# Kernel tuning notes

Hardware: AMD Instinct MI355X
Metric: run time of the kernel (lower is better)

## Reference

```python
import jax, jax.numpy as jnp
import numpy as np

B, N_P, N_S, D, H = 8, 512, 512, 512, 8
HD = D // H
SCALE = HD ** -0.5


def setup_inputs() -> dict:
    key = jax.random.key(0)
    ks = jax.random.split(key, 16)
    init = lambda k, shape, fan_in: jax.random.normal(k, shape, jnp.float32) * (1.0 / np.sqrt(fan_in))
    return {
        "piece_embeds": jax.random.normal(ks[0], (B, N_P, D), jnp.float32),
        "slot_embeds": jax.random.normal(ks[1], (B, N_S, D), jnp.float32),
        "mask": jax.random.randint(ks[2], (B, N_P, N_S), 0, 2, jnp.int32),
        "spatial_bias": jax.random.normal(ks[3], (B, N_P, N_S), jnp.float32),
        "Wq": init(ks[4], (D, D), D), "bq": jnp.zeros((D,), jnp.float32),
        "Wk": init(ks[5], (D, D), D), "bk": jnp.zeros((D,), jnp.float32),
        "Wv": init(ks[6], (D, D), D), "bv": jnp.zeros((D,), jnp.float32),
        "Wo": init(ks[7], (D, D), D), "bo": jnp.zeros((D,), jnp.float32),
        "Wc": init(ks[8], (2 * D,), 2 * D), "bc": jnp.zeros((), jnp.float32),
        "Wval": init(ks[9], (D,), D), "bval": jnp.zeros((), jnp.float32),
    }


def reference(piece_embeds, slot_embeds, mask, spatial_bias,
              Wq, bq, Wk, bk, Wv, bv, Wo, bo, Wc, bc, Wval, bval):
    Bv, Np, Dv = piece_embeds.shape
    Ns = slot_embeds.shape[1]
    Q = (piece_embeds @ Wq + bq).reshape(Bv, Np, H, HD)
    K = (slot_embeds @ Wk + bk).reshape(Bv, Ns, H, HD)
    V = (slot_embeds @ Wv + bv).reshape(Bv, Ns, H, HD)
    # per-head scores, scaled, then averaged over heads (non-standard)
    scores = jnp.einsum('bphd,bshd->bps', Q, K) * (SCALE / H)
    scores = scores + spatial_bias
    scores = jnp.where(mask == 0, jnp.float32(-1e9), scores)
    attn_probs = jax.nn.softmax(scores, axis=-1)  # dropout is identity at eval
    # the original expand*mul*sum over [B,Np,Ns,H,HD] == this contraction
    attn_output = jnp.einsum('bps,bshd->bphd', attn_probs, V).reshape(Bv, Np, Dv)
    output = attn_output @ Wo + bo
    value = (output.mean(axis=1) @ Wval + bval)[:, None]  # [B,1]
    # concat-linear over pairs == split-weight GEMMs with broadcast add
    Wc_p, Wc_s = Wc[:Dv], Wc[Dv:]
    compatibility = (piece_embeds @ Wc_p)[:, :, None] + (slot_embeds @ Wc_s)[:, None, :] + bc
    return scores, value, compatibility
```

## Files before the change

### kernel.cpp

```cpp
#include <hip/hip_runtime.h>
#include <math.h>

#define NP 512
#define NS 512
#define DD 512
#define INV64 0.015625f
#define NEGBIG -1000000000.0f
#define LOG2E 1.4426950408889634f

#define WS_MTBF   0
#define WS_TBF    131072
#define WS_PBF    1179648
#define WS_SBF    2228224
#define WS_WQBF   3276800
#define WS_WKBF   3407872
#define WS_WV     3538944
#define WS_U      3539456
#define WS_WQBK   3539968
#define WS_WKBQ   3540480
#define WS_VV     3540992
#define WS_A      3545088
#define WS_E      3549184
#define WS_CP     3553280
#define WS_CS     3557376
#define WS_Z      3561472
#define WS_W      3565568
#define WS_SC     3569664
#define WS_CNT    3569680

#define OUT_SCORES 0
#define OUT_VALUE  2097152
#define OUT_COMP   2097160

typedef short bf16x8 __attribute__((ext_vector_type(8)));
typedef float f32x4 __attribute__((ext_vector_type(4)));

__device__ __forceinline__ short f2bf(float f) {
  unsigned u = __builtin_bit_cast(unsigned, f);
  u += 0x7fffu + ((u >> 16) & 1u);
  return (short)(u >> 16);
}

__device__ __forceinline__ void async_copy16(const void* g, void* l) {
  __builtin_amdgcn_global_load_lds(
      (const __attribute__((address_space(1))) unsigned int*)g,
      (__attribute__((address_space(3))) unsigned int*)l, 16, 0, 0);
}

__device__ __forceinline__ float dot8(float4 a0, float4 a1, float4 b0, float4 b1) {
  return a0.x * b0.x + a0.y * b0.y + a0.z * b0.z + a0.w * b0.w +
         a1.x * b1.x + a1.y * b1.y + a1.z * b1.z + a1.w * b1.w;
}

__device__ __forceinline__ float wave_red(float s) {
#pragma unroll
  for (int o = 32; o; o >>= 1) s += __shfl_xor(s, o);
  return s;
}

__device__ inline float wave_dot512(const float* __restrict__ x,
                                    const float* __restrict__ y, int lane) {
  float4 x0 = *(const float4*)&x[lane * 8];
  float4 x1 = *(const float4*)&x[lane * 8 + 4];
  float4 y0 = *(const float4*)&y[lane * 8];
  float4 y1 = *(const float4*)&y[lane * 8 + 4];
  return wave_red(dot8(x0, x1, y0, y1));
}

__global__ __launch_bounds__(256) void kA(
    const float* __restrict__ Wo, const float* __restrict__ Wval,
    const float* __restrict__ Wq, const float* __restrict__ bk,
    const float* __restrict__ Wk, const float* __restrict__ bq,
    const float* __restrict__ bo, const float* __restrict__ bval,
    float* __restrict__ ws, short* __restrict__ wqb, short* __restrict__ wkb) {
  int blk = blockIdx.x;
  if (blk < 385) {
    int wid = blk * 4 + (threadIdx.x >> 6);
    int lane = threadIdx.x & 63;
    if (wid >= 1538) return;
    const float *x, *y;
    float* dst;
    float extra = 0.f;
    int r = wid & 511;
    if (wid < 512)        { x = Wo + (size_t)r * DD; y = Wval; dst = ws + WS_WV + r; }
    else if (wid < 1024)  { x = Wq + (size_t)r * DD; y = bk;   dst = ws + WS_WQBK + r; }
    else if (wid < 1536)  { x = Wk + (size_t)r * DD; y = bq;   dst = ws + WS_WKBQ + r; }
    else if (wid == 1536) { x = bo; y = Wval; dst = ws + WS_SC + 1; extra = *bval; }
    else                  { x = bq; y = bk;   dst = ws + WS_SC + 2; }
    float s = wave_dot512(x, y, lane);
    if (lane == 0) *dst = s + extra;
  } else {
    int t = (blk - 385) * 256 + threadIdx.x;
    const float* src;
    short* dst;
    int off;
    if (t < 32768) { src = Wq; dst = wqb; off = t * 8; }
    else           { src = Wk; dst = wkb; off = (t - 32768) * 8; }
    float4 v0 = *(const float4*)&src[off];
    float4 v1 = *(const float4*)&src[off + 4];
    bf16x8 o;
    o[0] = f2bf(v0.x); o[1] = f2bf(v0.y); o[2] = f2bf(v0.z); o[3] = f2bf(v0.w);
    o[4] = f2bf(v1.x); o[5] = f2bf(v1.y); o[6] = f2bf(v1.z); o[7] = f2bf(v1.w);
    *(bf16x8*)&dst[off] = o;
  }
}

template <int MODE>
__global__ __launch_bounds__(256) void k64(
    const short* __restrict__ A, const short* __restrict__ B,
    short* __restrict__ Cb, const float* __restrict__ Wv,
    const float* __restrict__ bv, float* __restrict__ ws,
    const float* __restrict__ sbias, const int* __restrict__ maskp,
    const float* __restrict__ bc, float* __restrict__ out) {
  __shared__ alignas(16) short SH[4][4096];
  __shared__ unsigned tick;
  const int wave = threadIdx.x >> 6, lane = threadIdx.x & 63;
  const int id = blockIdx.x;

  if (MODE == 0 && id >= 64) {
    int wid = (id - 64) * 4 + wave;
    if (wid > 512) return;
    if (wid < 512) {
      float s = wave_dot512(Wv + (size_t)wid * DD, ws + WS_WV, lane);
      if (lane == 0) ws[WS_U + wid] = s;
    } else {
      float s = wave_dot512(bv, ws + WS_WV, lane);
      if (lane == 0) ws[WS_SC + 0] = s;
    }
    return;
  }

  const int wr = wave >> 1, wc = wave & 1;
  const int li = lane & 15, g = lane >> 4;
  int b = 0, m0, n0;
  if (MODE == 0)      { m0 = (id & 7) * 64; n0 = (id >> 3) * 64; }
  else if (MODE == 1) { m0 = (id & 63) * 64; n0 = (id >> 6) * 64; }
  else                { b = id & 7; m0 = ((id >> 6) & 7) * 64; n0 = ((id >> 3) & 7) * 64; }
  const short* Ab = A + (size_t)b * NP * DD;
  const short* Bb = B + (size_t)b * NS * DD;
  f32x4 acc[2][2] = {};
  float4 sb4r[4];
  int4 mk4r[4];
  const int er = threadIdx.x >> 2, eq = threadIdx.x & 3;
  const size_t ebase = ((size_t)b * NP + m0 + er) * NS + n0 + eq * 16;

  auto stage = [&](int bufi, int k0) {
#pragma unroll
    for (int h = 0; h < 2; ++h) {
      int s = h * 256 + threadIdx.x;
      int row = s >> 3;
      int gsrc = (s & 7) ^ (row & 7);
      async_copy16(Ab + (size_t)(m0 + row) * DD + k0 + gsrc * 8, &SH[bufi][s * 8]);
      async_copy16(Bb + (size_t)(n0 + row) * DD + k0 + gsrc * 8, &SH[2 + bufi][s * 8]);
    }
  };

  stage(0, 0);
  __syncthreads();
  int buf = 0;
  for (int k0 = 0; k0 < DD; k0 += 64) {
    if (k0 + 64 < DD) stage(buf ^ 1, k0 + 64);
    if (MODE == 2) {
      if (k0 == 256) {
#pragma unroll
        for (int h = 0; h < 4; ++h)
          sb4r[h] = *(const float4*)&sbias[ebase + h * 4];
      } else if (k0 == 384) {
#pragma unroll
        for (int h = 0; h < 4; ++h)
          mk4r[h] = *(const int4*)&maskp[ebase + h * 4];
      }
    }
    bf16x8 af[2][2], bfv[2][2];
#pragma unroll
    for (int kk = 0; kk < 2; ++kk) {
#pragma unroll
      for (int am = 0; am < 2; ++am) {
        int row = wr * 32 + am * 16 + li;
        af[am][kk] = *(const bf16x8*)&SH[buf][(row * 8 + ((kk * 4 + g) ^ (row & 7))) * 8];
      }
#pragma unroll
      for (int bn = 0; bn < 2; ++bn) {
        int row = wc * 32 + bn * 16 + li;
        bfv[bn][kk] = *(const bf16x8*)&SH[2 + buf][(row * 8 + ((kk * 4 + g) ^ (row & 7))) * 8];
      }
    }
#pragma unroll
    for (int kk = 0; kk < 2; ++kk)
#pragma unroll
      for (int am = 0; am < 2; ++am)
#pragma unroll
        for (int bn = 0; bn < 2; ++bn)
          acc[am][bn] = __builtin_amdgcn_mfma_f32_16x16x32_bf16(
              af[am][kk], bfv[bn][kk], acc[am][bn], 0, 0, 0);
    if (k0 + 64 < DD) {
      __syncthreads();
      buf ^= 1;
    }
  }
  __syncthreads();

  if (MODE != 2) {
    short* cs = &SH[0][0];
#pragma unroll
    for (int am = 0; am < 2; ++am)
#pragma unroll
      for (int i = 0; i < 4; ++i) {
        int row = wr * 32 + am * 16 + g * 4 + i;
#pragma unroll
        for (int bn = 0; bn < 2; ++bn)
          cs[row * 68 + wc * 32 + bn * 16 + li] = f2bf(acc[am][bn][i]);
      }
    __syncthreads();
    int r = threadIdx.x >> 2, q = threadIdx.x & 3;
#pragma unroll
    for (int h = 0; h < 2; ++h) {
      bf16x8 v = *(const bf16x8*)&cs[r * 68 + q * 16 + h * 8];
      *(bf16x8*)&Cb[(size_t)(m0 + r) * DD + n0 + q * 16 + h * 8] = v;
    }
  } else {
    float* cf = (float*)&SH[0][0];
#pragma unroll
    for (int am = 0; am < 2; ++am)
#pragma unroll
      for (int i = 0; i < 4; ++i) {
        int row = wr * 32 + am * 16 + g * 4 + i;
#pragma unroll
        for (int bn = 0; bn < 2; ++bn)
          cf[row * 68 + wc * 32 + bn * 16 + li] = acc[am][bn][i];
      }
    __syncthreads();
    const float sbb = ws[WS_SC + 2];
    const float bcv = *bc;
    int p = m0 + er;
    float av = ws[WS_A + b * NP + p] + sbb;
    float cpv = ws[WS_CP + b * NP + p] + bcv;
    float zp = 0.f, wp = 0.f;
#pragma unroll
    for (int h = 0; h < 4; ++h) {
      int c = eq * 16 + h * 4;
      int scol = n0 + c;
      size_t idx = ebase + h * 4;
      float4 a4 = *(const float4*)&cf[er * 68 + c];
      float4 sb4 = sb4r[h];
      int4 mk4 = mk4r[h];
      float4 e4 = *(const float4*)&ws[WS_E + b * NS + scol];
      float4 vv4 = *(const float4*)&ws[WS_VV + b * NS + scol];
      float4 cs4 = *(const float4*)&ws[WS_CS + b * NS + scol];
      float4 v;
      v.x = (mk4.x == 0) ? NEGBIG : fmaf(a4.x + av + e4.x, INV64, sb4.x);
      v.y = (mk4.y == 0) ? NEGBIG : fmaf(a4.y + av + e4.y, INV64, sb4.y);
      v.z = (mk4.z == 0) ? NEGBIG : fmaf(a4.z + av + e4.z, INV64, sb4.z);
      v.w = (mk4.w == 0) ? NEGBIG : fmaf(a4.w + av + e4.w, INV64, sb4.w);
      *(float4*)&out[OUT_SCORES + idx] = v;
      float e;
      e = exp2f(v.x * LOG2E); zp += e; wp += e * vv4.x;
      e = exp2f(v.y * LOG2E); zp += e; wp += e * vv4.y;
      e = exp2f(v.z * LOG2E); zp += e; wp += e * vv4.z;
      e = exp2f(v.w * LOG2E); zp += e; wp += e * vv4.w;
      float4 cm = make_float4(cpv + cs4.x, cpv + cs4.y, cpv + cs4.z, cpv + cs4.w);
      *(float4*)&out[OUT_COMP + idx] = cm;
    }
    zp += __shfl_xor(zp, 1); zp += __shfl_xor(zp, 2);
    wp += __shfl_xor(wp, 1); wp += __shfl_xor(wp, 2);
    if (eq == 0) {
      atomicAdd(&ws[WS_Z + b * NP + p], zp);
      atomicAdd(&ws[WS_W + b * NP + p], wp);
    }
    __syncthreads();
    if (threadIdx.x == 0)
      tick = atomicAdd((unsigned*)(ws + WS_CNT) + (b * 8 + ((id >> 6) & 7)), 1u);
    __syncthreads();
    if (tick == 7 && threadIdx.x < 64) {
      int pr = m0 + threadIdx.x;
      float zz = atomicAdd(&ws[WS_Z + b * NP + pr], 0.0f);
      float ww = atomicAdd(&ws[WS_W + b * NP + pr], 0.0f);
      float v = wave_red(ww / zz);
      if (threadIdx.x == 0) atomicAdd(&out[OUT_VALUE + b], v * (1.0f / NP));
    }
  }
}

__global__ __launch_bounds__(256) void kC(
    const float* __restrict__ piece, const float* __restrict__ slot,
    const float* __restrict__ Wc, float* __restrict__ ws,
    short* __restrict__ pbf, short* __restrict__ sbf, float* __restrict__ out) {
  int lane = threadIdx.x & 63;
  if (blockIdx.x < 1024) {
    int wid = blockIdx.x * 4 + (threadIdx.x >> 6);
    const float* row = piece + (size_t)wid * DD;
    float4 x0 = *(const float4*)&row[lane * 8];
    float4 x1 = *(const float4*)&row[lane * 8 + 4];
    bf16x8 o;
    o[0] = f2bf(x0.x); o[1] = f2bf(x0.y); o[2] = f2bf(x0.z); o[3] = f2bf(x0.w);
    o[4] = f2bf(x1.x); o[5] = f2bf(x1.y); o[6] = f2bf(x1.z); o[7] = f2bf(x1.w);
    *(bf16x8*)&pbf[(size_t)wid * DD + lane * 8] = o;
    const float* y = ws + WS_WQBK;
    float4 y0 = *(const float4*)&y[lane * 8];
    float4 y1 = *(const float4*)&y[lane * 8 + 4];
    float4 c0 = *(const float4*)&Wc[lane * 8];
    float4 c1 = *(const float4*)&Wc[lane * 8 + 4];
    float da = wave_red(dot8(x0, x1, y0, y1));
    float dc = wave_red(dot8(x0, x1, c0, c1));
    if (lane == 0) { ws[WS_A + wid] = da; ws[WS_CP + wid] = dc; }
  } else if (blockIdx.x < 2048) {
    int wid = (blockIdx.x - 1024) * 4 + (threadIdx.x >> 6);
    const float* row = slot + (size_t)wid * DD;
    float4 x0 = *(const float4*)&row[lane * 8];
    float4 x1 = *(const float4*)&row[lane * 8 + 4];
    bf16x8 o;
    o[0] = f2bf(x0.x); o[1] = f2bf(x0.y); o[2] = f2bf(x0.z); o[3] = f2bf(x0.w);
    o[4] = f2bf(x1.x); o[5] = f2bf(x1.y); o[6] = f2bf(x1.z); o[7] = f2bf(x1.w);
    *(bf16x8*)&sbf[(size_t)wid * DD + lane * 8] = o;
    const float* y = ws + WS_WKBQ;
    float4 y0 = *(const float4*)&y[lane * 8];
    float4 y1 = *(const float4*)&y[lane * 8 + 4];
    const float* u = ws + WS_U;
    float4 u0 = *(const float4*)&u[lane * 8];
    float4 u1 = *(const float4*)&u[lane * 8 + 4];
    const float* c = Wc + DD;
    float4 c0 = *(const float4*)&c[lane * 8];
    float4 c1 = *(const float4*)&c[lane * 8 + 4];
    float de = wave_red(dot8(x0, x1, y0, y1));
    float dv = wave_red(dot8(x0, x1, u0, u1));
    float dc = wave_red(dot8(x0, x1, c0, c1));
    if (lane == 0) {
      ws[WS_E + wid] = de;
      ws[WS_VV + wid] = dv + ws[WS_SC + 0];
      ws[WS_CS + wid] = dc;
    }
  } else {
    float4 zz = make_float4(0.f, 0.f, 0.f, 0.f);
#pragma unroll
    for (int k = 0; k < 8; ++k)
      *(float4*)&ws[WS_Z + (threadIdx.x * 8 + k) * 4] = zz;
    if (threadIdx.x < 64) ((unsigned*)(ws + WS_CNT))[threadIdx.x] = 0u;
    if (threadIdx.x < 8) out[OUT_VALUE + threadIdx.x] = ws[WS_SC + 1];
  }
}

extern "C" void kernel_launch(void* const* d_in, const int* in_sizes, int n_in,
                              void* d_out, int out_size, void* d_ws,
                              size_t ws_size, hipStream_t stream) {
  const float* piece = (const float*)d_in[0];
  const float* slot = (const float*)d_in[1];
  const int* mask = (const int*)d_in[2];
  const float* sbias = (const float*)d_in[3];
  const float* Wq = (const float*)d_in[4];
  const float* bq = (const float*)d_in[5];
  const float* Wk = (const float*)d_in[6];
  const float* bk = (const float*)d_in[7];
  const float* Wv = (const float*)d_in[8];
  const float* bv = (const float*)d_in[9];
  const float* Wo = (const float*)d_in[10];
  const float* bo = (const float*)d_in[11];
  const float* Wc = (const float*)d_in[12];
  const float* bc = (const float*)d_in[13];
  const float* Wval = (const float*)d_in[14];
  const float* bval = (const float*)d_in[15];
  float* out = (float*)d_out;
  float* ws = (float*)d_ws;

  short* mtb = (short*)(ws + WS_MTBF);
  short* tbf = (short*)(ws + WS_TBF);
  short* pbf = (short*)(ws + WS_PBF);
  short* sbf = (short*)(ws + WS_SBF);
  short* wqb = (short*)(ws + WS_WQBF);
  short* wkb = (short*)(ws + WS_WKBF);

  hipLaunchKernelGGL(kA, dim3(641), dim3(256), 0, stream,
                     Wo, Wval, Wq, bk, Wk, bq, bo, bval, ws, wqb, wkb);
  hipLaunchKernelGGL((k64<0>), dim3(193), dim3(256), 0, stream,
                     wkb, wqb, mtb, Wv, bv, ws,
                     (const float*)nullptr, (const int*)nullptr,
                     (const float*)nullptr, (float*)nullptr);
  hipLaunchKernelGGL(kC, dim3(2049), dim3(256), 0, stream, piece, slot, Wc, ws,
                     pbf, sbf, out);
  hipLaunchKernelGGL((k64<1>), dim3(512), dim3(256), 0, stream,
                     pbf, mtb, tbf, (const float*)nullptr, (const float*)nullptr,
                     ws, (const float*)nullptr, (const int*)nullptr,
                     (const float*)nullptr, (float*)nullptr);
  hipLaunchKernelGGL((k64<2>), dim3(512), dim3(256), 0, stream,
                     tbf, sbf, (short*)nullptr, (const float*)nullptr,
                     (const float*)nullptr, ws, sbias, mask, bc, out);
}
```

Baseline: 45.07 us.

## Fuse weight bf16 conversion into Wk·Wqᵀ GEMM and rebalance stage kernels

The separate pass that converted Wq and Wk to bf16 in workspace is dropped. The Wk·Wqᵀ GEMM now loads fp32 tiles, converts them in registers and stages them in padded shared memory, and is merged into the first kernel. The slot-embedding conversion and its dot products move into extra blocks of the piece·M GEMM launch, and the Wv·wv dot products move into the piece-conversion kernel. This cuts one launch and the bf16 weight round trip through memory. In exchange, the fused GEMM loads synchronously instead of through async LDS copies, and it writes uncoalesced scalar bf16 outputs.

```diff
diff --git a/kernel.cpp b/kernel.cpp
--- a/kernel.cpp
+++ b/kernel.cpp
@@ -12,8 +12,6 @@
 #define WS_TBF    131072
 #define WS_PBF    1179648
 #define WS_SBF    2228224
-#define WS_WQBF   3276800
-#define WS_WKBF   3407872
 #define WS_WV     3538944
 #define WS_U      3539456
 #define WS_WQBK   3539968
@@ -41,6 +39,13 @@
   return (short)(u >> 16);
 }
 
+__device__ __forceinline__ bf16x8 cvt8(float4 a, float4 b) {
+  bf16x8 o;
+  o[0] = f2bf(a.x); o[1] = f2bf(a.y); o[2] = f2bf(a.z); o[3] = f2bf(a.w);
+  o[4] = f2bf(b.x); o[5] = f2bf(b.y); o[6] = f2bf(b.z); o[7] = f2bf(b.w);
+  return o;
+}
+
 __device__ __forceinline__ void async_copy16(const void* g, void* l) {
   __builtin_amdgcn_global_load_lds(
       (const __attribute__((address_space(1))) unsigned int*)g,
@@ -67,12 +72,14 @@
   return wave_red(dot8(x0, x1, y0, y1));
 }
 
-__global__ __launch_bounds__(256) void kA(
+__global__ __launch_bounds__(256) void kAM(
     const float* __restrict__ Wo, const float* __restrict__ Wval,
     const float* __restrict__ Wq, const float* __restrict__ bk,
     const float* __restrict__ Wk, const float* __restrict__ bq,
     const float* __restrict__ bo, const float* __restrict__ bval,
-    float* __restrict__ ws, short* __restrict__ wqb, short* __restrict__ wkb) {
+    float* __restrict__ ws, short* __restrict__ mtb) {
+  __shared__ alignas(16) short Asw[2][64 * 72];
+  __shared__ alignas(16) short Bsw[2][64 * 72];
   int blk = blockIdx.x;
   if (blk < 385) {
     int wid = blk * 4 + (threadIdx.x >> 6);
@@ -89,36 +96,92 @@
     else                  { x = bq; y = bk;   dst = ws + WS_SC + 2; }
     float s = wave_dot512(x, y, lane);
     if (lane == 0) *dst = s + extra;
-  } else {
-    int t = (blk - 385) * 256 + threadIdx.x;
-    const float* src;
-    short* dst;
-    int off;
-    if (t < 32768) { src = Wq; dst = wqb; off = t * 8; }
-    else           { src = Wk; dst = wkb; off = (t - 32768) * 8; }
-    float4 v0 = *(const float4*)&src[off];
-    float4 v1 = *(const float4*)&src[off + 4];
+    return;
+  }
+  int gb = blk - 385;
+  const int m0 = (gb & 7) * 64, n0 = (gb >> 3) * 64;
+  const int wave = threadIdx.x >> 6, lane = threadIdx.x & 63;
+  const int wr = wave >> 1, wc = wave & 1;
+  const int li = lane & 15, g = lane >> 4;
+  const int arow = threadIdx.x >> 2, aseg = threadIdx.x & 3;
+  f32x4 acc[2][2] = {};
+
+  auto stage = [&](int bufi, int k0) {
+    const float* sa = Wk + (size_t)(m0 + arow) * DD + k0 + aseg * 16;
+    float4 a0 = *(const float4*)sa, a1 = *(const float4*)(sa + 4);
+    float4 a2 = *(const float4*)(sa + 8), a3 = *(const float4*)(sa + 12);
+    const float* sb = Wq + (size_t)(n0 + arow) * DD + k0 + aseg * 16;
+    float4 b0 = *(const float4*)sb, b1 = *(const float4*)(sb + 4);
+    float4 b2 = *(const float4*)(sb + 8), b3 = *(const float4*)(sb + 12);
+    *(bf16x8*)&Asw[bufi][arow * 72 + aseg * 16] = cvt8(a0, a1);
+    *(bf16x8*)&Asw[bufi][arow * 72 + aseg * 16 + 8] = cvt8(a2, a3);
+    *(bf16x8*)&Bsw[bufi][arow * 72 + aseg * 16] = cvt8(b0, b1);
+    *(bf16x8*)&Bsw[bufi][arow * 72 + aseg * 16 + 8] = cvt8(b2, b3);
+  };
+
+  stage(0, 0);
+  __syncthreads();
+  int buf = 0;
+  for (int k0 = 0; k0 < DD; k0 += 64) {
+    if (k0 + 64 < DD) stage(buf ^ 1, k0 + 64);
+    bf16x8 af[2][2], bfv[2][2];
+#pragma unroll
+    for (int kk = 0; kk < 2; ++kk) {
+#pragma unroll
+      for (int am = 0; am < 2; ++am)
+        af[am][kk] = *(const bf16x8*)&Asw[buf][(wr * 32 + am * 16 + li) * 72 + kk * 32 + g * 8];
+#pragma unroll
+      for (int bn = 0; bn < 2; ++bn)
+        bfv[bn][kk] = *(const bf16x8*)&Bsw[buf][(wc * 32 + bn * 16 + li) * 72 + kk * 32 + g * 8];
+    }
+#pragma unroll
+    for (int kk = 0; kk < 2; ++kk)
+#pragma unroll
+      for (int am = 0; am < 2; ++am)
+#pragma unroll
+        for (int bn = 0; bn < 2; ++bn)
+          acc[am][bn] = __builtin_amdgcn_mfma_f32_16x16x32_bf16(
+              af[am][kk], bfv[bn][kk], acc[am][bn], 0, 0, 0);
+    __syncthreads();
+    buf ^= 1;
+  }
+#pragma unroll
+  for (int am = 0; am < 2; ++am)
+#pragma unroll
+    for (int i = 0; i < 4; ++i) {
+      int grow = m0 + wr * 32 + am * 16 + g * 4 + i;
+#pragma unroll
+      for (int bn = 0; bn < 2; ++bn) {
+        int gcol = n0 + wc * 32 + bn * 16 + li;
+        mtb[(size_t)grow * DD + gcol] = f2bf(acc[am][bn][i]);
+      }
+    }
+}
+
+__global__ __launch_bounds__(256) void kCp(
+    const float* __restrict__ piece, const float* __restrict__ Wv,
+    const float* __restrict__ bv, const float* __restrict__ Wc,
+    float* __restrict__ ws, short* __restrict__ pbf, float* __restrict__ out) {
+  int lane = threadIdx.x & 63;
+  if (blockIdx.x < 1024) {
+    int wid = blockIdx.x * 4 + (threadIdx.x >> 6);
+    const float* row = piece + (size_t)wid * DD;
+    float4 x0 = *(const float4*)&row[lane * 8];
+    float4 x1 = *(const float4*)&row[lane * 8 + 4];
     bf16x8 o;
-    o[0] = f2bf(v0.x); o[1] = f2bf(v0.y); o[2] = f2bf(v0.z); o[3] = f2bf(v0.w);
-    o[4] = f2bf(v1.x); o[5] = f2bf(v1.y); o[6] = f2bf(v1.z); o[7] = f2bf(v1.w);
-    *(bf16x8*)&dst[off] = o;
-  }
-}
-
-template <int MODE>
-__global__ __launch_bounds__(256) void k64(
-    const short* __restrict__ A, const short* __restrict__ B,
-    short* __restrict__ Cb, const float* __restrict__ Wv,
-    const float* __restrict__ bv, float* __restrict__ ws,
-    const float* __restrict__ sbias, const int* __restrict__ maskp,
-    const float* __restrict__ bc, float* __restrict__ out) {
-  __shared__ alignas(16) short SH[4][4096];
-  __shared__ unsigned tick;
-  const int wave = threadIdx.x >> 6, lane = threadIdx.x & 63;
-  const int id = blockIdx.x;
-
-  if (MODE == 0 && id >= 64) {
-    int wid = (id - 64) * 4 + wave;
+    o[0] = f2bf(x0.x); o[1] = f2bf(x0.y); o[2] = f2bf(x0.z); o[3] = f2bf(x0.w);
+    o[4] = f2bf(x1.x); o[5] = f2bf(x1.y); o[6] = f2bf(x1.z); o[7] = f2bf(x1.w);
+    *(bf16x8*)&pbf[(size_t)wid * DD + lane * 8] = o;
+    const float* y = ws + WS_WQBK;
+    float4 y0 = *(const float4*)&y[lane * 8];
+    float4 y1 = *(const float4*)&y[lane * 8 + 4];
+    float4 c0 = *(const float4*)&Wc[lane * 8];
+    float4 c1 = *(const float4*)&Wc[lane * 8 + 4];
+    float da = wave_red(dot8(x0, x1, y0, y1));
+    float dc = wave_red(dot8(x0, x1, c0, c1));
+    if (lane == 0) { ws[WS_A + wid] = da; ws[WS_CP + wid] = dc; }
+  } else if (blockIdx.x < 1153) {
+    int wid = ((int)blockIdx.x - 1024) * 4 + (threadIdx.x >> 6);
     if (wid > 512) return;
     if (wid < 512) {
       float s = wave_dot512(Wv + (size_t)wid * DD, ws + WS_WV, lane);
@@ -127,15 +190,63 @@
       float s = wave_dot512(bv, ws + WS_WV, lane);
       if (lane == 0) ws[WS_SC + 0] = s;
     }
+  } else {
+    float4 zz = make_float4(0.f, 0.f, 0.f, 0.f);
+#pragma unroll
+    for (int k = 0; k < 8; ++k)
+      *(float4*)&ws[WS_Z + (threadIdx.x * 8 + k) * 4] = zz;
+    if (threadIdx.x < 64) ((unsigned*)(ws + WS_CNT))[threadIdx.x] = 0u;
+    if (threadIdx.x < 8) out[OUT_VALUE + threadIdx.x] = ws[WS_SC + 1];
+  }
+}
+
+template <int MODE>
+__global__ __launch_bounds__(256) void k64(
+    const short* __restrict__ A, const short* __restrict__ B,
+    short* __restrict__ Cb, const float* __restrict__ slotp,
+    const float* __restrict__ Wc, float* __restrict__ ws,
+    const float* __restrict__ sbias, const int* __restrict__ maskp,
+    const float* __restrict__ bc, float* __restrict__ out,
+    short* __restrict__ sbf) {
+  __shared__ alignas(16) short SH[4][4096];
+  __shared__ unsigned tick;
+  const int wave = threadIdx.x >> 6, lane = threadIdx.x & 63;
+  const int id = blockIdx.x;
+
+  if (MODE == 1 && id >= 512) {
+    int wid = (id - 512) * 4 + wave;
+    const float* row = slotp + (size_t)wid * DD;
+    float4 x0 = *(const float4*)&row[lane * 8];
+    float4 x1 = *(const float4*)&row[lane * 8 + 4];
+    bf16x8 o;
+    o[0] = f2bf(x0.x); o[1] = f2bf(x0.y); o[2] = f2bf(x0.z); o[3] = f2bf(x0.w);
+    o[4] = f2bf(x1.x); o[5] = f2bf(x1.y); o[6] = f2bf(x1.z); o[7] = f2bf(x1.w);
+    *(bf16x8*)&sbf[(size_t)wid * DD + lane * 8] = o;
+    const float* y = ws + WS_WKBQ;
+    float4 y0 = *(const float4*)&y[lane * 8];
+    float4 y1 = *(const float4*)&y[lane * 8 + 4];
+    const float* u = ws + WS_U;
+    float4 u0 = *(const float4*)&u[lane * 8];
+    float4 u1 = *(const float4*)&u[lane * 8 + 4];
+    const float* c = Wc + DD;
+    float4 c0 = *(const float4*)&c[lane * 8];
+    float4 c1 = *(const float4*)&c[lane * 8 + 4];
+    float de = wave_red(dot8(x0, x1, y0, y1));
+    float dv = wave_red(dot8(x0, x1, u0, u1));
+    float dc = wave_red(dot8(x0, x1, c0, c1));
+    if (lane == 0) {
+      ws[WS_E + wid] = de;
+      ws[WS_VV + wid] = dv + ws[WS_SC + 0];
+      ws[WS_CS + wid] = dc;
+    }
     return;
   }
 
   const int wr = wave >> 1, wc = wave & 1;
   const int li = lane & 15, g = lane >> 4;
   int b = 0, m0, n0;
-  if (MODE == 0)      { m0 = (id & 7) * 64; n0 = (id >> 3) * 64; }
-  else if (MODE == 1) { m0 = (id & 63) * 64; n0 = (id >> 6) * 64; }
-  else                { b = id & 7; m0 = ((id >> 6) & 7) * 64; n0 = ((id >> 3) & 7) * 64; }
+  if (MODE == 1) { m0 = (id & 63) * 64; n0 = (id >> 6) * 64; }
+  else           { b = id & 7; m0 = ((id >> 6) & 7) * 64; n0 = ((id >> 3) & 7) * 64; }
   const short* Ab = A + (size_t)b * NP * DD;
   const short* Bb = B + (size_t)b * NS * DD;
   f32x4 acc[2][2] = {};
@@ -200,7 +311,7 @@
   }
   __syncthreads();
 
-  if (MODE != 2) {
+  if (MODE == 1) {
     short* cs = &SH[0][0];
 #pragma unroll
     for (int am = 0; am < 2; ++am)
@@ -281,64 +392,6 @@
   }
 }
 
-__global__ __launch_bounds__(256) void kC(
-    const float* __restrict__ piece, const float* __restrict__ slot,
-    const float* __restrict__ Wc, float* __restrict__ ws,
-    short* __restrict__ pbf, short* __restrict__ sbf, float* __restrict__ out) {
-  int lane = threadIdx.x & 63;
-  if (blockIdx.x < 1024) {
-    int wid = blockIdx.x * 4 + (threadIdx.x >> 6);
-    const float* row = piece + (size_t)wid * DD;
-    float4 x0 = *(const float4*)&row[lane * 8];
-    float4 x1 = *(const float4*)&row[lane * 8 + 4];
-    bf16x8 o;
-    o[0] = f2bf(x0.x); o[1] = f2bf(x0.y); o[2] = f2bf(x0.z); o[3] = f2bf(x0.w);
-    o[4] = f2bf(x1.x); o[5] = f2bf(x1.y); o[6] = f2bf(x1.z); o[7] = f2bf(x1.w);
-    *(bf16x8*)&pbf[(size_t)wid * DD + lane * 8] = o;
-    const float* y = ws + WS_WQBK;
-    float4 y0 = *(const float4*)&y[lane * 8];
-    float4 y1 = *(const float4*)&y[lane * 8 + 4];
-    float4 c0 = *(const float4*)&Wc[lane * 8];
-    float4 c1 = *(const float4*)&Wc[lane * 8 + 4];
-    float da = wave_red(dot8(x0, x1, y0, y1));
-    float dc = wave_red(dot8(x0, x1, c0, c1));
-    if (lane == 0) { ws[WS_A + wid] = da; ws[WS_CP + wid] = dc; }
-  } else if (blockIdx.x < 2048) {
-    int wid = (blockIdx.x - 1024) * 4 + (threadIdx.x >> 6);
-    const float* row = slot + (size_t)wid * DD;
-    float4 x0 = *(const float4*)&row[lane * 8];
-    float4 x1 = *(const float4*)&row[lane * 8 + 4];
-    bf16x8 o;
-    o[0] = f2bf(x0.x); o[1] = f2bf(x0.y); o[2] = f2bf(x0.z); o[3] = f2bf(x0.w);
-    o[4] = f2bf(x1.x); o[5] = f2bf(x1.y); o[6] = f2bf(x1.z); o[7] = f2bf(x1.w);
-    *(bf16x8*)&sbf[(size_t)wid * DD + lane * 8] = o;
-    const float* y = ws + WS_WKBQ;
-    float4 y0 = *(const float4*)&y[lane * 8];
-    float4 y1 = *(const float4*)&y[lane * 8 + 4];
-    const float* u = ws + WS_U;
-    float4 u0 = *(const float4*)&u[lane * 8];
-    float4 u1 = *(const float4*)&u[lane * 8 + 4];
-    const float* c = Wc + DD;
-    float4 c0 = *(const float4*)&c[lane * 8];
-    float4 c1 = *(const float4*)&c[lane * 8 + 4];
-    float de = wave_red(dot8(x0, x1, y0, y1));
-    float dv = wave_red(dot8(x0, x1, u0, u1));
-    float dc = wave_red(dot8(x0, x1, c0, c1));
-    if (lane == 0) {
-      ws[WS_E + wid] = de;
-      ws[WS_VV + wid] = dv + ws[WS_SC + 0];
-      ws[WS_CS + wid] = dc;
-    }
-  } else {
-    float4 zz = make_float4(0.f, 0.f, 0.f, 0.f);
-#pragma unroll
-    for (int k = 0; k < 8; ++k)
-      *(float4*)&ws[WS_Z + (threadIdx.x * 8 + k) * 4] = zz;
-    if (threadIdx.x < 64) ((unsigned*)(ws + WS_CNT))[threadIdx.x] = 0u;
-    if (threadIdx.x < 8) out[OUT_VALUE + threadIdx.x] = ws[WS_SC + 1];
-  }
-}
-
 extern "C" void kernel_launch(void* const* d_in, const int* in_sizes, int n_in,
                               void* d_out, int out_size, void* d_ws,
                               size_t ws_size, hipStream_t stream) {
@@ -365,22 +418,17 @@
   short* tbf = (short*)(ws + WS_TBF);
   short* pbf = (short*)(ws + WS_PBF);
   short* sbf = (short*)(ws + WS_SBF);
-  short* wqb = (short*)(ws + WS_WQBF);
-  short* wkb = (short*)(ws + WS_WKBF);
-
-  hipLaunchKernelGGL(kA, dim3(641), dim3(256), 0, stream,
-                     Wo, Wval, Wq, bk, Wk, bq, bo, bval, ws, wqb, wkb);
-  hipLaunchKernelGGL((k64<0>), dim3(193), dim3(256), 0, stream,
-                     wkb, wqb, mtb, Wv, bv, ws,
+
+  hipLaunchKernelGGL(kAM, dim3(449), dim3(256), 0, stream,
+                     Wo, Wval, Wq, bk, Wk, bq, bo, bval, ws, mtb);
+  hipLaunchKernelGGL(kCp, dim3(1154), dim3(256), 0, stream,
+                     piece, Wv, bv, Wc, ws, pbf, out);
+  hipLaunchKernelGGL((k64<1>), dim3(1536), dim3(256), 0, stream,
+                     pbf, mtb, tbf, slot, Wc, ws,
                      (const float*)nullptr, (const int*)nullptr,
-                     (const float*)nullptr, (float*)nullptr);
-  hipLaunchKernelGGL(kC, dim3(2049), dim3(256), 0, stream, piece, slot, Wc, ws,
-                     pbf, sbf, out);
-  hipLaunchKernelGGL((k64<1>), dim3(512), dim3(256), 0, stream,
-                     pbf, mtb, tbf, (const float*)nullptr, (const float*)nullptr,
-                     ws, (const float*)nullptr, (const int*)nullptr,
-                     (const float*)nullptr, (float*)nullptr);
+                     (const float*)nullptr, (float*)nullptr, sbf);
   hipLaunchKernelGGL((k64<2>), dim3(512), dim3(256), 0, stream,
                      tbf, sbf, (short*)nullptr, (const float*)nullptr,
-                     (const float*)nullptr, ws, sbias, mask, bc, out);
-}
+                     (const float*)nullptr, ws, sbias, mask, bc, out,
+                     (short*)nullptr);
+}
```

Measured after the change: 43.11 us, median of 2. -4.3%, faster.
